# Kernel tuning notes

Hardware: AMD Instinct MI355X
Metric: run time of the kernel (lower is better)

The kernel has to match this reference:

```python
import jax, jax.numpy as jnp
import numpy as np

H = 16           # num_heads
D = 1024         # num_units
QD = KD = VD = 64
LN_EPS = 1e-5


def _xavier(key, shape):
    fan_in, fan_out = shape[-2], shape[-1]
    std = np.sqrt(2.0 / (fan_in + fan_out))
    return jax.random.normal(key, shape, dtype=jnp.float32) * std


def setup_inputs() -> dict:
    key = jax.random.key(0)
    ks = jax.random.split(key, 10)
    B, Sq, Sk = 8, 1024, 1024
    return {
        "query": jax.random.normal(ks[0], (B, Sq, D), dtype=jnp.float32),
        "keys": jax.random.normal(ks[1], (B, Sk, D), dtype=jnp.float32),
        "values": jax.random.normal(ks[2], (B, Sk, D), dtype=jnp.float32),
        "Wq": _xavier(ks[3], (H, D, QD)),
        "Wk": _xavier(ks[4], (H, D, KD)),
        "Wv": _xavier(ks[5], (H, D, VD)),
        "Wp": _xavier(ks[6], (H * VD, D)),   # proj, stored input-major: y = x @ Wp + bp
        "bp": jnp.zeros((D,), dtype=jnp.float32),
        "gamma": jnp.ones((D,), dtype=jnp.float32),
        "beta": jnp.zeros((D,), dtype=jnp.float32),
    }


def reference(query, keys, values, Wq, Wk, Wv, Wp, bp, gamma, beta):
    B, Sq, _ = query.shape
    Sk = keys.shape[1]
    # RepeatLinear per head: [B,S,D] x [H,D,e] -> [H,B,S,e]
    Q = jnp.einsum("bsd,hde->hbse", query, Wq)
    K = jnp.einsum("bsd,hde->hbse", keys, Wk)
    V = jnp.einsum("bsd,hde->hbse", values, Wv)
    # NOTE: original scales by sqrt(num_units), not sqrt(key_dim)
    temper = jnp.asarray(np.sqrt(D), dtype=Q.dtype)
    scores = jnp.einsum("hbqe,hbke->hbqk", Q, K) / temper  # [H,B,Sq,Sk]
    attn = jax.nn.softmax(scores, axis=-1)
    # dropout is identity in eval mode
    out = jnp.einsum("hbqk,hbke->hbqe", attn, V)           # [H,B,Sq,VD]
    # torch.cat(torch.split(out, B, 0), -1): head-major feature concat
    out = out.transpose(1, 2, 0, 3).reshape(B, Sq, H * VD)
    out = out @ Wp + bp                                     # proj
    # residual + LayerNorm
    y = out + query
    mu = jnp.mean(y, axis=-1, keepdims=True)
    var = jnp.var(y, axis=-1, keepdims=True)
    y = (y - mu) / jnp.sqrt(var + LN_EPS) * gamma + beta
    return y, attn.reshape(H * B, Sq, Sk)
```

## Files before the change

### kernel.cpp

```cpp
#include <hip/hip_runtime.h>
#include <hip/hip_bf16.h>

#define H_ 16
#define B_ 8
#define S_ 1024
#define D_ 1024
#define E_ 64
#define HB_ 128
#define LN_EPS 1e-5f

typedef unsigned short u16;
typedef __bf16 bf16x8 __attribute__((ext_vector_type(8)));
typedef u16 u16x8 __attribute__((ext_vector_type(8)));
typedef u16 u16x4 __attribute__((ext_vector_type(4)));
typedef float f32x4 __attribute__((ext_vector_type(4)));

#define MFMA16(a, b, c) __builtin_amdgcn_mfma_f32_16x16x32_bf16( \
    __builtin_bit_cast(bf16x8, (a)), __builtin_bit_cast(bf16x8, (b)), (c), 0, 0, 0)

#define GLL16(gp, lp) __builtin_amdgcn_global_load_lds( \
    (const __attribute__((address_space(1))) void*)(gp), \
    (__attribute__((address_space(3))) void*)(lp), 16, 0, 0)

__device__ __forceinline__ u16 f2bf(float x) {
  union { float f; unsigned u; } v; v.f = x;
  unsigned r = v.u + 0x7fffu + ((v.u >> 16) & 1u);
  return (u16)(r >> 16);
}

__global__ __launch_bounds__(256) void k_transpose_tile(const float* __restrict__ in,
    u16* __restrict__ out, int R, int C, float scale) {
  __shared__ float tile[64][65];
  const int rt = blockIdx.x * 64, ct = blockIdx.y * 64;
  const size_t so = (size_t)blockIdx.z * R * C;
  const float* I = in + so;
  u16* O = out + so;
  const int t = threadIdx.x;
  const int c4 = (t & 15) * 4;
  #pragma unroll
  for (int i = 0; i < 4; i++) {
    int r = i * 16 + (t >> 4);
    f32x4 v = *(const f32x4*)&I[(size_t)(rt + r) * C + ct + c4];
    tile[r][c4 + 0] = v[0]; tile[r][c4 + 1] = v[1];
    tile[r][c4 + 2] = v[2]; tile[r][c4 + 3] = v[3];
  }
  __syncthreads();
  #pragma unroll
  for (int i = 0; i < 4; i++) {
    int oc = i * 16 + (t >> 4);
    u16x4 v;
    #pragma unroll
    for (int r = 0; r < 4; r++) v[r] = f2bf(tile[c4 + r][oc] * scale);
    *(u16x4*)&O[(size_t)(ct + oc) * R + rt + c4] = v;
  }
}

__global__ void k_convert(const float* __restrict__ X, u16* __restrict__ Y) {
  int i = (blockIdx.x * 256 + threadIdx.x) * 8;
  float4 a = *(const float4*)(X + i);
  float4 b = *(const float4*)(X + i + 4);
  u16x8 v;
  v[0] = f2bf(a.x); v[1] = f2bf(a.y); v[2] = f2bf(a.z); v[3] = f2bf(a.w);
  v[4] = f2bf(b.x); v[5] = f2bf(b.y); v[6] = f2bf(b.z); v[7] = f2bf(b.w);
  *(u16x8*)(Y + i) = v;
}

template<int MODE>
__global__ __launch_bounds__(256) void k_gemm(
    const u16* __restrict__ X0, const u16* __restrict__ X1,
    const u16* __restrict__ Ball,
    u16* __restrict__ O0, u16* __restrict__ O1,
    float* __restrict__ Pf, const float* __restrict__ bp,
    const float* __restrict__ query) {
  const int bid = blockIdx.x + (blockIdx.y << 6);
  const int bx  = ((bid & 7) << 3) + ((bid >> 3) & 7);
  const int by  = bid >> 6;
  const int l  = threadIdx.x & 63;
  const int w  = threadIdx.x >> 6;
  const int lr = l & 15, lg = l >> 4;
  const int wr = w >> 1, wc = w & 1;
  const int m0 = bx * 128, n0 = by * 128;

  const u16* A = (MODE == 0 && by >= 8) ? X1 : X0;

  __shared__ __align__(16) u16 As[128 * 32];
  __shared__ __align__(16) u16 Bs[128 * 32];

  const int srow = w * 16 + (l >> 2);
  const int scol = (l & 3) * 8;
  const u16* Ag = A    + (size_t)(m0 + srow) * 1024 + scol;
  const u16* Bg = Ball + (size_t)(n0 + srow) * 1024 + scol;
  u16* AsB0 = As + w * 512;
  u16* BsB0 = Bs + w * 512;

  f32x4 acc[4][4] = {};

  for (int kt = 0; kt < 1024; kt += 32) {
    GLL16(Ag + kt,             AsB0);
    GLL16(Ag + 64 * 1024 + kt, AsB0 + 2048);
    GLL16(Bg + kt,             BsB0);
    GLL16(Bg + 64 * 1024 + kt, BsB0 + 2048);
    __syncthreads();

    u16x8 af[4], bf[4];
    #pragma unroll
    for (int mi = 0; mi < 4; mi++)
      af[mi] = *(const u16x8*)&As[(wr * 64 + mi * 16 + lr) * 32 + lg * 8];
    #pragma unroll
    for (int ni = 0; ni < 4; ni++)
      bf[ni] = *(const u16x8*)&Bs[(wc * 64 + ni * 16 + lr) * 32 + lg * 8];

    #pragma unroll
    for (int mi = 0; mi < 4; mi++)
      #pragma unroll
      for (int ni = 0; ni < 4; ni++) {
        if (MODE == 1) acc[mi][ni] = MFMA16(af[mi], bf[ni], acc[mi][ni]);
        else           acc[mi][ni] = MFMA16(bf[ni], af[mi], acc[mi][ni]);
      }
    __syncthreads();
  }

  if (MODE == 0) {
    u16* Out = (by >= 8) ? O1 : O0;
    const int h = (by & 7) * 2 + wc;
    #pragma unroll
    for (int mi = 0; mi < 4; mi++) {
      int s = m0 + wr * 64 + mi * 16 + lr;
      int bb = s >> 10, ss = s & 1023;
      #pragma unroll
      for (int ni = 0; ni < 4; ni++) {
        u16x4 v;
        #pragma unroll
        for (int r = 0; r < 4; r++) v[r] = f2bf(acc[mi][ni][r]);
        *(u16x4*)&Out[((size_t)(h * 8 + bb) * 1024 + ss) * 64 + ni * 16 + lg * 4] = v;
      }
    }
  } else if (MODE == 1) {
    const int h = by * 2 + wc;
    #pragma unroll
    for (int mi = 0; mi < 4; mi++) {
      int s = m0 + wr * 64 + mi * 16 + lg * 4;
      int bb = s >> 10, ss = s & 1023;
      #pragma unroll
      for (int ni = 0; ni < 4; ni++) {
        u16x4 v;
        #pragma unroll
        for (int r = 0; r < 4; r++) v[r] = f2bf(acc[mi][ni][r]);
        *(u16x4*)&O0[((size_t)(h * 8 + bb) * 64 + ni * 16 + lr) * 1024 + ss] = v;
      }
    }
  } else {
    #pragma unroll
    for (int mi = 0; mi < 4; mi++) {
      int m = m0 + wr * 64 + mi * 16 + lr;
      #pragma unroll
      for (int ni = 0; ni < 4; ni++) {
        int n = n0 + wc * 64 + ni * 16 + lg * 4;
        f32x4 b4 = *(const f32x4*)(bp + n);
        f32x4 q4 = *(const f32x4*)(query + (size_t)m * 1024 + n);
        f32x4 o = acc[mi][ni] + b4 + q4;
        *(f32x4*)(Pf + (size_t)m * 1024 + n) = o;
      }
    }
  }
}

__global__ __launch_bounds__(256, 4) void k_attn(const u16* __restrict__ Qb,
    const u16* __restrict__ Kb, const u16* __restrict__ Vtb,
    float* __restrict__ attn_out, u16* __restrict__ AO) {
  const int bid = blockIdx.x;
  const int xcd = bid & 7, within = bid >> 3;
  const int qt = within & 63;
  const int hb = xcd * 16 + (within >> 6);
  const int w  = threadIdx.x >> 6;
  const int l  = threadIdx.x & 63;
  const int lr = l & 15, lg = l >> 4;
  const int q0 = qt * 16;

  __shared__ __align__(16) u16 pbuf[16 * 1024];
  __shared__ float wmaxs[4][16];
  __shared__ float wsums[4][16];

  const u16* Qp = Qb + ((size_t)hb * 1024 + q0 + lr) * 64 + lg * 8;
  const u16* Kp = Kb + ((size_t)hb * 1024 + w * 256 + lr) * 64 + lg * 8;
  u16x8 q_lo = *(const u16x8*)Qp;
  u16x8 q_hi = *(const u16x8*)(Qp + 32);

  f32x4 sacc[16] = {};
  #pragma unroll
  for (int j = 0; j < 16; j++) {
    u16x8 k0 = *(const u16x8*)(Kp + (size_t)j * 16 * 64);
    u16x8 k1 = *(const u16x8*)(Kp + (size_t)j * 16 * 64 + 32);
    sacc[j] = MFMA16(k0, q_lo, sacc[j]);
    sacc[j] = MFMA16(k1, q_hi, sacc[j]);
  }

  float mx = sacc[0][0];
  #pragma unroll
  for (int j = 0; j < 16; j++)
    #pragma unroll
    for (int r = 0; r < 4; r++) mx = fmaxf(mx, sacc[j][r]);
  mx = fmaxf(mx, __shfl_xor(mx, 16));
  mx = fmaxf(mx, __shfl_xor(mx, 32));

  float sum = 0.f;
  #pragma unroll
  for (int j = 0; j < 16; j++)
    #pragma unroll
    for (int r = 0; r < 4; r++) {
      float p = __expf(sacc[j][r] - mx);
      sacc[j][r] = p;
      sum += p;
    }
  sum += __shfl_xor(sum, 16);
  sum += __shfl_xor(sum, 32);

  #pragma unroll
  for (int j = 0; j < 16; j++) {
    u16x4 pb;
    #pragma unroll
    for (int r = 0; r < 4; r++) pb[r] = f2bf(sacc[j][r]);
    int k0 = w * 256 + j * 16 + lg * 4;
    int byte = (lr * 2048 + k0 * 2) ^ ((lr & 7) << 4);
    *(u16x4*)((char*)pbuf + byte) = pb;
  }
  if (l < 16) { wmaxs[w][lr] = mx; wsums[w][lr] = sum; }

  __syncthreads();

  float m0v = wmaxs[0][lr], m1v = wmaxs[1][lr], m2v = wmaxs[2][lr], m3v = wmaxs[3][lr];
  float gmax = fmaxf(fmaxf(m0v, m1v), fmaxf(m2v, m3v));
  float e0 = __expf(m0v - gmax), e1 = __expf(m1v - gmax);
  float e2 = __expf(m2v - gmax), e3 = __expf(m3v - gmax);
  float gsum = wsums[0][lr] * e0 + wsums[1][lr] * e1 + wsums[2][lr] * e2 + wsums[3][lr] * e3;
  float inv = 1.0f / gsum;
  float c0 = e0 * inv, c1 = e1 * inv, c2 = e2 * inv, c3 = e3 * inv;
  float scale_own = __expf(mx - gmax) * inv;

  float* Ap = attn_out + ((size_t)hb * 1024 + q0 + lr) * 1024 + w * 256 + lg * 4;
  #pragma unroll
  for (int j = 0; j < 16; j++) {
    f32x4 v = sacc[j] * scale_own;
    __builtin_nontemporal_store(v, (f32x4*)(Ap + j * 16));
  }

  const u16* Vp = Vtb + ((size_t)hb * 64 + w * 16 + lr) * 1024 + lg * 8;
  f32x4 o0 = {}, o1 = {}, o2 = {}, o3 = {};
  #pragma unroll
  for (int i = 0; i < 4; i++)
    #pragma unroll
    for (int kk = 0; kk < 8; kk++) {
      int kb = i * 256 + kk * 32 + lg * 8;
      int byte = (lr * 2048 + kb * 2) ^ ((lr & 7) << 4);
      u16x8 p = *(u16x8*)((char*)pbuf + byte);
      u16x8 v = *(const u16x8*)(Vp + i * 256 + kk * 32);
      if (i == 0) o0 = MFMA16(v, p, o0);
      else if (i == 1) o1 = MFMA16(v, p, o1);
      else if (i == 2) o2 = MFMA16(v, p, o2);
      else o3 = MFMA16(v, p, o3);
    }

  const int bb = hb & 7, hh = hb >> 3;
  u16x4 ov;
  #pragma unroll
  for (int r = 0; r < 4; r++)
    ov[r] = f2bf(o0[r] * c0 + o1[r] * c1 + o2[r] * c2 + o3[r] * c3);
  *(u16x4*)&AO[((size_t)bb * 1024 + q0 + lr) * 1024 + hh * 64 + w * 16 + lg * 4] = ov;
}

__global__ __launch_bounds__(256) void k_ln(const float* __restrict__ P,
    const float* __restrict__ gamma, const float* __restrict__ beta,
    float* __restrict__ y) {
  const int row = blockIdx.x * 4 + (threadIdx.x >> 6);
  const int l = threadIdx.x & 63;
  const float* p = P + (size_t)row * 1024 + l * 4;
  f32x4 v[4];
  float s = 0.f, s2 = 0.f;
  #pragma unroll
  for (int i = 0; i < 4; i++) {
    v[i] = *(const f32x4*)(p + i * 256);
    #pragma unroll
    for (int r = 0; r < 4; r++) { s += v[i][r]; s2 += v[i][r] * v[i][r]; }
  }
  #pragma unroll
  for (int off = 1; off < 64; off <<= 1) {
    s += __shfl_xor(s, off);
    s2 += __shfl_xor(s2, off);
  }
  float mu = s * (1.0f / 1024.0f);
  float var = s2 * (1.0f / 1024.0f) - mu * mu;
  float rstd = rsqrtf(var + LN_EPS);
  float* yp = y + (size_t)row * 1024 + l * 4;
  #pragma unroll
  for (int i = 0; i < 4; i++) {
    f32x4 g = *(const f32x4*)(gamma + l * 4 + i * 256);
    f32x4 b = *(const f32x4*)(beta + l * 4 + i * 256);
    f32x4 o;
    #pragma unroll
    for (int r = 0; r < 4; r++) o[r] = (v[i][r] - mu) * rstd * g[r] + b[r];
    __builtin_nontemporal_store(o, (f32x4*)(yp + i * 256));
  }
}

extern "C" void kernel_launch(void* const* d_in, const int* in_sizes, int n_in,
                              void* d_out, int out_size, void* d_ws, size_t ws_size,
                              hipStream_t stream) {
  const float* query  = (const float*)d_in[0];
  const float* keys   = (const float*)d_in[1];
  const float* values = (const float*)d_in[2];
  const float* Wq     = (const float*)d_in[3];
  const float* Wk     = (const float*)d_in[4];
  const float* Wv     = (const float*)d_in[5];
  const float* Wp     = (const float*)d_in[6];
  const float* bp     = (const float*)d_in[7];
  const float* gamma  = (const float*)d_in[8];
  const float* beta   = (const float*)d_in[9];

  float* y        = (float*)d_out;
  float* attn_out = (float*)d_out + (size_t)B_ * S_ * D_;

  u16* ws  = (u16*)d_ws;
  u16* Wqt = ws;
  u16* Wkt = Wqt + (1 << 20);
  u16* Wvt = Wkt + (1 << 20);
  u16* Wpt = Wvt + (1 << 20);
  u16* Xqb = Wpt + (1 << 20);
  u16* Xkb = Xqb + (8 << 20);
  u16* Xvb = Xkb + (8 << 20);
  u16* Qb  = Xvb + (8 << 20);
  u16* Kb  = Qb + (8 << 20);
  u16* Vtb = Kb + (8 << 20);
  u16* AO  = Vtb + (8 << 20);
  float* P = (float*)Xqb;

  k_transpose_tile<<<dim3(16, 1, 16), 256, 0, stream>>>(Wq, Wqt, 1024, 64, 1.0f / 32.0f);
  k_transpose_tile<<<dim3(16, 1, 16), 256, 0, stream>>>(Wk, Wkt, 1024, 64, 1.0f);
  k_transpose_tile<<<dim3(16, 1, 16), 256, 0, stream>>>(Wv, Wvt, 1024, 64, 1.0f);
  k_transpose_tile<<<dim3(16, 16, 1), 256, 0, stream>>>(Wp, Wpt, 1024, 1024, 1.0f);
  k_convert<<<4096, 256, 0, stream>>>(query,  Xqb);
  k_convert<<<4096, 256, 0, stream>>>(keys,   Xkb);
  k_convert<<<4096, 256, 0, stream>>>(values, Xvb);

  k_gemm<0><<<dim3(64, 16), 256, 0, stream>>>(Xqb, Xkb, Wqt, Qb, Kb, nullptr, nullptr, nullptr);
  k_gemm<1><<<dim3(64, 8),  256, 0, stream>>>(Xvb, nullptr, Wvt, Vtb, nullptr, nullptr, nullptr, nullptr);

  k_attn<<<8192, 256, 0, stream>>>(Qb, Kb, Vtb, attn_out, AO);

  k_gemm<2><<<dim3(64, 8),  256, 0, stream>>>(AO, nullptr, Wpt, nullptr, nullptr, P, bp, query);
  k_ln<<<2048, 256, 0, stream>>>(P, gamma, beta, y);
}
```

Measured before the change: 440.3 us.

## Merge preprocessing and QKV projection launches; prefetch V and raise MFMA priority in attention

Folds the four weight-transpose launches into one kernel and the three fp32-to-bf16 converts into one, then runs the Q, K and V projections as a single GEMM launch over 24 column-tile rows, using a contiguous workspace layout. This cuts launch count and lets the V projection share a wave with Q/K instead of running as a separate small grid. In the attention kernel, the first V fragments are loaded before softmax finishes, and s_setprio wraps the MFMA loops. Together these aim to reduce launch overhead and tail effects and to hide V load latency, at the cost of more branching and register pressure.

```diff
diff --git a/kernel.cpp b/kernel.cpp
--- a/kernel.cpp
+++ b/kernel.cpp
@@ -28,21 +28,39 @@
   return (u16)(r >> 16);
 }
 
-__global__ __launch_bounds__(256) void k_transpose_tile(const float* __restrict__ in,
-    u16* __restrict__ out, int R, int C, float scale) {
+__global__ __launch_bounds__(256) void k_transpose_all(
+    const float* __restrict__ Wq, const float* __restrict__ Wk,
+    const float* __restrict__ Wv, const float* __restrict__ Wp,
+    u16* __restrict__ Wt) {
   __shared__ float tile[64][65];
-  const int rt = blockIdx.x * 64, ct = blockIdx.y * 64;
-  const size_t so = (size_t)blockIdx.z * R * C;
-  const float* I = in + so;
-  u16* O = out + so;
+  const int bid = blockIdx.x;
+  const int which = bid >> 8, r = bid & 255;
+  const float* src;
+  int R, C, rt, ct;
+  float scale = 1.0f;
+  size_t soff, doff;
+  if (which < 3) {
+    src = which == 0 ? Wq : which == 1 ? Wk : Wv;
+    if (which == 0) scale = 1.0f / 32.0f;
+    int slice = r & 15, rtile = r >> 4;
+    R = 1024; C = 64; rt = rtile * 64; ct = 0;
+    soff = (size_t)slice * 65536;
+    doff = (size_t)which * (1 << 20) + (size_t)slice * 65536;
+  } else {
+    src = Wp;
+    R = 1024; C = 1024; rt = (r & 15) * 64; ct = (r >> 4) * 64;
+    soff = 0; doff = (size_t)3 * (1 << 20);
+  }
+  const float* I = src + soff;
+  u16* O = Wt + doff;
   const int t = threadIdx.x;
   const int c4 = (t & 15) * 4;
   #pragma unroll
   for (int i = 0; i < 4; i++) {
-    int r = i * 16 + (t >> 4);
-    f32x4 v = *(const f32x4*)&I[(size_t)(rt + r) * C + ct + c4];
-    tile[r][c4 + 0] = v[0]; tile[r][c4 + 1] = v[1];
-    tile[r][c4 + 2] = v[2]; tile[r][c4 + 3] = v[3];
+    int rr = i * 16 + (t >> 4);
+    f32x4 v = *(const f32x4*)&I[(size_t)(rt + rr) * C + ct + c4];
+    tile[rr][c4 + 0] = v[0]; tile[rr][c4 + 1] = v[1];
+    tile[rr][c4 + 2] = v[2]; tile[rr][c4 + 3] = v[3];
   }
   __syncthreads();
   #pragma unroll
@@ -50,13 +68,18 @@
     int oc = i * 16 + (t >> 4);
     u16x4 v;
     #pragma unroll
-    for (int r = 0; r < 4; r++) v[r] = f2bf(tile[c4 + r][oc] * scale);
+    for (int rr = 0; rr < 4; rr++) v[rr] = f2bf(tile[c4 + rr][oc] * scale);
     *(u16x4*)&O[(size_t)(ct + oc) * R + rt + c4] = v;
   }
 }
 
-__global__ void k_convert(const float* __restrict__ X, u16* __restrict__ Y) {
-  int i = (blockIdx.x * 256 + threadIdx.x) * 8;
+__global__ void k_convert3(const float* __restrict__ Xq, const float* __restrict__ Xk,
+    const float* __restrict__ Xv, u16* __restrict__ dst) {
+  const int bid = blockIdx.x;
+  const int t = bid >> 12;
+  const float* X = t == 0 ? Xq : t == 1 ? Xk : Xv;
+  u16* Y = dst + (size_t)t * (8 << 20);
+  int i = ((bid & 4095) * 256 + threadIdx.x) * 8;
   float4 a = *(const float4*)(X + i);
   float4 b = *(const float4*)(X + i + 4);
   u16x8 v;
@@ -65,11 +88,26 @@
   *(u16x8*)(Y + i) = v;
 }
 
+#define STAGE_TILES() do { \
+    GLL16(Ag + kt,             AsB0); \
+    GLL16(Ag + 64 * 1024 + kt, AsB0 + 2048); \
+    GLL16(Bg + kt,             BsB0); \
+    GLL16(Bg + 64 * 1024 + kt, BsB0 + 2048); \
+  } while (0)
+
+#define READ_FRAGS() do { \
+    _Pragma("unroll") \
+    for (int mi = 0; mi < 4; mi++) \
+      af[mi] = *(const u16x8*)&As[(wr * 64 + mi * 16 + lr) * 32 + lg * 8]; \
+    _Pragma("unroll") \
+    for (int ni = 0; ni < 4; ni++) \
+      bf[ni] = *(const u16x8*)&Bs[(wc * 64 + ni * 16 + lr) * 32 + lg * 8]; \
+  } while (0)
+
 template<int MODE>
 __global__ __launch_bounds__(256) void k_gemm(
-    const u16* __restrict__ X0, const u16* __restrict__ X1,
-    const u16* __restrict__ Ball,
-    u16* __restrict__ O0, u16* __restrict__ O1,
+    const u16* __restrict__ X0, const u16* __restrict__ Ball,
+    u16* __restrict__ O0, u16* __restrict__ O1, u16* __restrict__ O2,
     float* __restrict__ Pf, const float* __restrict__ bp,
     const float* __restrict__ query) {
   const int bid = blockIdx.x + (blockIdx.y << 6);
@@ -81,7 +119,7 @@
   const int wr = w >> 1, wc = w & 1;
   const int m0 = bx * 128, n0 = by * 128;
 
-  const u16* A = (MODE == 0 && by >= 8) ? X1 : X0;
+  const u16* A = (MODE == 0) ? X0 + (size_t)(by >> 3) * (8 << 20) : X0;
 
   __shared__ __align__(16) u16 As[128 * 32];
   __shared__ __align__(16) u16 Bs[128 * 32];
@@ -94,33 +132,35 @@
   u16* BsB0 = Bs + w * 512;
 
   f32x4 acc[4][4] = {};
-
-  for (int kt = 0; kt < 1024; kt += 32) {
-    GLL16(Ag + kt,             AsB0);
-    GLL16(Ag + 64 * 1024 + kt, AsB0 + 2048);
-    GLL16(Bg + kt,             BsB0);
-    GLL16(Bg + 64 * 1024 + kt, BsB0 + 2048);
-    __syncthreads();
-
-    u16x8 af[4], bf[4];
-    #pragma unroll
-    for (int mi = 0; mi < 4; mi++)
-      af[mi] = *(const u16x8*)&As[(wr * 64 + mi * 16 + lr) * 32 + lg * 8];
-    #pragma unroll
-    for (int ni = 0; ni < 4; ni++)
-      bf[ni] = *(const u16x8*)&Bs[(wc * 64 + ni * 16 + lr) * 32 + lg * 8];
-
-    #pragma unroll
-    for (int mi = 0; mi < 4; mi++)
-      #pragma unroll
-      for (int ni = 0; ni < 4; ni++) {
-        if (MODE == 1) acc[mi][ni] = MFMA16(af[mi], bf[ni], acc[mi][ni]);
-        else           acc[mi][ni] = MFMA16(bf[ni], af[mi], acc[mi][ni]);
-      }
-    __syncthreads();
-  }
-
-  if (MODE == 0) {
+  u16x8 af[4], bf[4];
+
+  if (MODE == 2 || by < 16) {
+    for (int kt = 0; kt < 1024; kt += 32) {
+      STAGE_TILES();
+      __syncthreads();
+      READ_FRAGS();
+      #pragma unroll
+      for (int mi = 0; mi < 4; mi++)
+        #pragma unroll
+        for (int ni = 0; ni < 4; ni++)
+          acc[mi][ni] = MFMA16(bf[ni], af[mi], acc[mi][ni]);
+      __syncthreads();
+    }
+  } else {
+    for (int kt = 0; kt < 1024; kt += 32) {
+      STAGE_TILES();
+      __syncthreads();
+      READ_FRAGS();
+      #pragma unroll
+      for (int mi = 0; mi < 4; mi++)
+        #pragma unroll
+        for (int ni = 0; ni < 4; ni++)
+          acc[mi][ni] = MFMA16(af[mi], bf[ni], acc[mi][ni]);
+      __syncthreads();
+    }
+  }
+
+  if (MODE == 0 && by < 16) {
     u16* Out = (by >= 8) ? O1 : O0;
     const int h = (by & 7) * 2 + wc;
     #pragma unroll
@@ -135,8 +175,9 @@
         *(u16x4*)&Out[((size_t)(h * 8 + bb) * 1024 + ss) * 64 + ni * 16 + lg * 4] = v;
       }
     }
-  } else if (MODE == 1) {
-    const int h = by * 2 + wc;
+  } else if (MODE == 0) {
+    const int byv = by - 16;
+    const int h = byv * 2 + wc;
     #pragma unroll
     for (int mi = 0; mi < 4; mi++) {
       int s = m0 + wr * 64 + mi * 16 + lg * 4;
@@ -146,7 +187,7 @@
         u16x4 v;
         #pragma unroll
         for (int r = 0; r < 4; r++) v[r] = f2bf(acc[mi][ni][r]);
-        *(u16x4*)&O0[((size_t)(h * 8 + bb) * 64 + ni * 16 + lr) * 1024 + ss] = v;
+        *(u16x4*)&O2[((size_t)(h * 8 + bb) * 64 + ni * 16 + lr) * 1024 + ss] = v;
       }
     }
   } else {
@@ -187,6 +228,7 @@
   u16x8 q_hi = *(const u16x8*)(Qp + 32);
 
   f32x4 sacc[16] = {};
+  __builtin_amdgcn_s_setprio(1);
   #pragma unroll
   for (int j = 0; j < 16; j++) {
     u16x8 k0 = *(const u16x8*)(Kp + (size_t)j * 16 * 64);
@@ -194,6 +236,7 @@
     sacc[j] = MFMA16(k0, q_lo, sacc[j]);
     sacc[j] = MFMA16(k1, q_hi, sacc[j]);
   }
+  __builtin_amdgcn_s_setprio(0);
 
   float mx = sacc[0][0];
   #pragma unroll
@@ -214,6 +257,12 @@
     }
   sum += __shfl_xor(sum, 16);
   sum += __shfl_xor(sum, 32);
+
+  const u16* Vp = Vtb + ((size_t)hb * 64 + w * 16 + lr) * 1024 + lg * 8;
+  u16x8 vp0 = *(const u16x8*)(Vp + 0);
+  u16x8 vp1 = *(const u16x8*)(Vp + 32);
+  u16x8 vp2 = *(const u16x8*)(Vp + 64);
+  u16x8 vp3 = *(const u16x8*)(Vp + 96);
 
   #pragma unroll
   for (int j = 0; j < 16; j++) {
@@ -244,8 +293,8 @@
     __builtin_nontemporal_store(v, (f32x4*)(Ap + j * 16));
   }
 
-  const u16* Vp = Vtb + ((size_t)hb * 64 + w * 16 + lr) * 1024 + lg * 8;
   f32x4 o0 = {}, o1 = {}, o2 = {}, o3 = {};
+  __builtin_amdgcn_s_setprio(1);
   #pragma unroll
   for (int i = 0; i < 4; i++)
     #pragma unroll
@@ -253,12 +302,18 @@
       int kb = i * 256 + kk * 32 + lg * 8;
       int byte = (lr * 2048 + kb * 2) ^ ((lr & 7) << 4);
       u16x8 p = *(u16x8*)((char*)pbuf + byte);
-      u16x8 v = *(const u16x8*)(Vp + i * 256 + kk * 32);
+      u16x8 v;
+      if (i == 0 && kk == 0) v = vp0;
+      else if (i == 0 && kk == 1) v = vp1;
+      else if (i == 0 && kk == 2) v = vp2;
+      else if (i == 0 && kk == 3) v = vp3;
+      else v = *(const u16x8*)(Vp + i * 256 + kk * 32);
       if (i == 0) o0 = MFMA16(v, p, o0);
       else if (i == 1) o1 = MFMA16(v, p, o1);
       else if (i == 2) o2 = MFMA16(v, p, o2);
       else o3 = MFMA16(v, p, o3);
     }
+  __builtin_amdgcn_s_setprio(0);
 
   const int bb = hb & 7, hh = hb >> 3;
   u16x4 ov;
@@ -321,31 +376,24 @@
 
   u16* ws  = (u16*)d_ws;
   u16* Wqt = ws;
-  u16* Wkt = Wqt + (1 << 20);
-  u16* Wvt = Wkt + (1 << 20);
-  u16* Wpt = Wvt + (1 << 20);
-  u16* Xqb = Wpt + (1 << 20);
-  u16* Xkb = Xqb + (8 << 20);
-  u16* Xvb = Xkb + (8 << 20);
-  u16* Qb  = Xvb + (8 << 20);
+  u16* Wvt = Wqt + (2 << 20);
+  u16* Wpt = Wqt + (3 << 20);
+  u16* Xqb = Wqt + (4 << 20);
+  u16* Xvb = Xqb + (16 << 20);
+  u16* Qb  = Xqb + (24 << 20);
   u16* Kb  = Qb + (8 << 20);
   u16* Vtb = Kb + (8 << 20);
   u16* AO  = Vtb + (8 << 20);
   float* P = (float*)Xqb;
-
-  k_transpose_tile<<<dim3(16, 1, 16), 256, 0, stream>>>(Wq, Wqt, 1024, 64, 1.0f / 32.0f);
-  k_transpose_tile<<<dim3(16, 1, 16), 256, 0, stream>>>(Wk, Wkt, 1024, 64, 1.0f);
-  k_transpose_tile<<<dim3(16, 1, 16), 256, 0, stream>>>(Wv, Wvt, 1024, 64, 1.0f);
-  k_transpose_tile<<<dim3(16, 16, 1), 256, 0, stream>>>(Wp, Wpt, 1024, 1024, 1.0f);
-  k_convert<<<4096, 256, 0, stream>>>(query,  Xqb);
-  k_convert<<<4096, 256, 0, stream>>>(keys,   Xkb);
-  k_convert<<<4096, 256, 0, stream>>>(values, Xvb);
-
-  k_gemm<0><<<dim3(64, 16), 256, 0, stream>>>(Xqb, Xkb, Wqt, Qb, Kb, nullptr, nullptr, nullptr);
-  k_gemm<1><<<dim3(64, 8),  256, 0, stream>>>(Xvb, nullptr, Wvt, Vtb, nullptr, nullptr, nullptr, nullptr);
+  (void)Wvt;
+
+  k_transpose_all<<<1024, 256, 0, stream>>>(Wq, Wk, Wv, Wp, Wqt);
+  k_convert3<<<12288, 256, 0, stream>>>(query, keys, values, Xqb);
+
+  k_gemm<0><<<dim3(64, 24), 256, 0, stream>>>(Xqb, Wqt, Qb, Kb, Vtb, nullptr, nullptr, nullptr);
 
   k_attn<<<8192, 256, 0, stream>>>(Qb, Kb, Vtb, attn_out, AO);
 
-  k_gemm<2><<<dim3(64, 8),  256, 0, stream>>>(AO, nullptr, Wpt, nullptr, nullptr, P, bp, query);
+  k_gemm<2><<<dim3(64, 8), 256, 0, stream>>>(AO, Wpt, nullptr, nullptr, nullptr, P, bp, query);
   k_ln<<<2048, 256, 0, stream>>>(P, gamma, beta, y);
 }
```

Result: faster. 421.9 us (-4.2%).
